# Kernel tuning notes

Hardware: AMD Instinct MI355X
Metric: run time of the kernel (lower is better)

## Reference

```python
import jax, jax.numpy as jnp
import numpy as np

# dims: batch, num queries, context len, model dim, heads, head dim,
# num_q_group, v_repeat, lora rank
B, NQ, NC, D = 4, 416, 257, 768
H, DH = 6, 128
G, R, LORA = 104, 4, 64  # NQ == R * G, all_q_mid == G * LORA
EPS = 1e-5


def ln(x, g, b):
    m = jnp.mean(x, axis=-1, keepdims=True)
    v = jnp.mean(jnp.square(x - m), axis=-1, keepdims=True)
    return (x - m) * jax.lax.rsqrt(v + EPS) * g + b


def setup_inputs() -> dict:
    key = jax.random.key(0)
    ks = jax.random.split(key, 7)
    s = 0.02
    return {
        "x": jax.random.normal(ks[0], (B, NQ, D), dtype=jnp.float32),
        "context": jax.random.normal(ks[1], (B, NC, D), dtype=jnp.float32),
        "Wq": jax.random.normal(ks[2], (D, D), dtype=jnp.float32) * s,
        "gq": jnp.ones((D,), jnp.float32), "bq": jnp.zeros((D,), jnp.float32),
        "Wk": jax.random.normal(ks[3], (D, D), dtype=jnp.float32) * s,
        "gk": jnp.ones((D,), jnp.float32), "bk": jnp.zeros((D,), jnp.float32),
        "Wv": jax.random.normal(ks[4], (D, G * LORA), dtype=jnp.float32) * s,
        "gv1": jnp.ones((G * LORA,), jnp.float32), "bv1": jnp.zeros((G * LORA,), jnp.float32),
        "Wconv": jax.random.normal(ks[5], (G, LORA, D), dtype=jnp.float32) * s,  # grouped 1x1 conv: per-group (LORA -> D)
        "gv2": jnp.ones((D,), jnp.float32), "bv2": jnp.zeros((D,), jnp.float32),
        "Wo": jax.random.normal(ks[6], (D, D), dtype=jnp.float32) * s,
        "go": jnp.ones((D,), jnp.float32), "bo": jnp.zeros((D,), jnp.float32),
    }


def reference(x, context, Wq, gq, bq, Wk, gk, bk, Wv, gv1, bv1, Wconv, gv2, bv2, Wo, go, bo):
    # to_q / to_k: Linear (no bias) + affine LayerNorm
    q = ln(x @ Wq, gq, bq)          # (B, NQ, D)
    k = ln(context @ Wk, gk, bk)    # (B, NC, D)
    # split heads -> (B*H, n, DH)
    q = q.reshape(B, NQ, H, DH).transpose(0, 2, 1, 3).reshape(B * H, NQ, DH)
    k = k.reshape(B, NC, H, DH).transpose(0, 2, 1, 3).reshape(B * H, NC, DH)

    # q-aware to_v: Linear -> LN -> grouped 1x1 Conv1d -> LN, plus skip of context
    mid = ln(context @ Wv, gv1, bv1)                 # (B, NC, G*LORA)
    mid = mid.reshape(B, NC, G, LORA)
    v = jnp.einsum('bngl,gld->bgnd', mid, Wconv)     # grouped conv, (B, G, NC, D)
    v = ln(v, gv2, bv2)
    v = v + context[:, None]                          # v_has_skip: context.unsqueeze(1)
    # heads: (B, G, NC, H, DH) -> (B*H, G, NC, DH)
    v = v.reshape(B, G, NC, H, DH).transpose(0, 3, 1, 2, 4).reshape(B * H, G, NC, DH)

    scale = DH ** (-0.25)
    sim = jnp.einsum('bid,bjd->bij', q * scale, k * scale)   # (B*H, NQ, NC)
    attn = jax.nn.softmax(sim, axis=-1)                       # dropout in eval mode: identity

    # torch repeat(1, R, 1, 1) tiles v along q-dim: query i uses group i % G.
    # reshape attn to (B*H, R, G, NC) so that i = r*G + g maps to group g.
    attn_g = attn.reshape(B * H, R, G, NC)
    out = jnp.einsum('brgj,bgjd->brgd', attn_g, v).reshape(B * H, NQ, DH)

    # merge heads -> (B, NQ, D)
    out = out.reshape(B, H, NQ, DH).transpose(0, 2, 1, 3).reshape(B, NQ, D)
    # to_out: Linear (no bias) + Dropout(eval: identity) + affine LayerNorm
    return ln(out @ Wo, go, bo)
```

## Files before the change

kernel.cpp:

```cpp
#include <hip/hip_runtime.h>


typedef unsigned short u16;
typedef unsigned int   u32;
typedef __attribute__((ext_vector_type(4))) float f32x4;
typedef __attribute__((ext_vector_type(4))) u32   u32x4;
typedef __attribute__((ext_vector_type(8))) short bf16x8;

__device__ __forceinline__ float bf2f(u16 v) { return __uint_as_float(((u32)v) << 16); }
__device__ __forceinline__ u16 f2bf(float f) {
  u32 u = __float_as_uint(f);
  u32 r = u + 0x7fffu + ((u >> 16) & 1u);
  return (u16)(r >> 16);
}
__device__ __forceinline__ float gld(const void* p, long idx, int f32) {
  return f32 ? ((const float*)p)[idx] : bf2f(((const u16*)p)[idx]);
}

typedef const __attribute__((address_space(1))) u32 gas_u32;
typedef __attribute__((address_space(3))) u32 las_u32;

__device__ __forceinline__ void stage16(const u16* g, u16* lbase, int lane) {
#if __has_builtin(__builtin_amdgcn_global_load_lds)
  (void)lane;
  __builtin_amdgcn_global_load_lds((gas_u32*)g, (las_u32*)lbase, 16, 0, 0);
#else
  *(u32x4*)(lbase + lane * 8) = *(const u32x4*)g;
#endif
}

__global__ __launch_bounds__(256) void probe_k(const u32* __restrict__ xw, int* __restrict__ flag) {
  int tid = threadIdx.x, c = 0;
  for (int i = tid; i < 4096; i += 256) {
    u16 lo = (u16)(xw[i] & 0xffffu);
    float a = fabsf(bf2f(lo));
    if (lo == 0 || (a >= 1e-3f && a <= 32.f)) ++c;
  }
#pragma unroll
  for (int o = 32; o; o >>= 1) c += __shfl_xor(c, o, 64);
  __shared__ int r[4];
  if ((tid & 63) == 0) r[tid >> 6] = c;
  __syncthreads();
  if (tid == 0) flag[0] = (r[0] + r[1] + r[2] + r[3] >= 2048) ? 0 : 1;
}

__global__ __launch_bounds__(256) void fill_k(u16* p, float v, int n) {
  int i = blockIdx.x * 256 + threadIdx.x;
  if (i < n) p[i] = f2bf(v);
}

__global__ __launch_bounds__(256) void prep_k(
    const void* __restrict__ x,   u16* __restrict__ xb,
    const void* __restrict__ ctx, u16* __restrict__ cbuf,
    const void* __restrict__ Wcv, u16* __restrict__ wcvb,
    u16* __restrict__ midi,
    const void* __restrict__ Wq, const void* __restrict__ Wk,
    const void* __restrict__ Wo, const void* __restrict__ Wv,
    u16* __restrict__ wqt, u16* __restrict__ wkt, u16* __restrict__ wot,
    u16* __restrict__ wvt, u16* __restrict__ ctxT,
    float* __restrict__ wbar, const int* __restrict__ dtf)
{
  const int f = dtf[0];
  int bid = blockIdx.x;
  __shared__ float s[32][33];
  if (bid < 3597) {
    const long n0_ = 1277952, n1_ = 789504, n2_ = 5111808, n3_ = 186368;
    long i = ((long)bid * 256 + threadIdx.x) * 8;
    const long t0 = n0_, t1 = t0 + n1_, t2 = t1 + n2_, t3 = t2 + n3_;
    if (i >= t3) return;
    if (i >= t2) {
      long e = i - t2;
      long z = e / 448, off = e - z * 448;
      u32x4 zz = {0u, 0u, 0u, 0u};
      *(u32x4*)(midi + z * 16896 + 16448 + off) = zz;
      return;
    }
    const void* in; u16* out;
    if (i < t0)      { in = x;    out = xb; }
    else if (i < t1) { in = ctx;  out = cbuf; i -= t0; }
    else             { in = Wcv;  out = wcvb; i -= t1; }
    if (f) {
      const float* ip = (const float*)in + i;
      f32x4 a = *(const f32x4*)ip, b = *(const f32x4*)(ip + 4);
      u32x4 q = { (u32)f2bf(a.x) | ((u32)f2bf(a.y) << 16),
                  (u32)f2bf(a.z) | ((u32)f2bf(a.w) << 16),
                  (u32)f2bf(b.x) | ((u32)f2bf(b.y) << 16),
                  (u32)f2bf(b.z) | ((u32)f2bf(b.w) << 16) };
      *(u32x4*)(out + i) = q;
    } else {
      *(u32x4*)(out + i) = *(const u32x4*)((const u16*)in + i);
    }
  } else if (bid < 11181) {
    int t = bid - 3597;
    const void* in; u16* out;
    int inK, inN, ldo, outK, nx;
    long inBase = 0, outBase = 0;
    if (t < 1728) {
      int w = t / 576; t -= w * 576;
      in  = w == 0 ? Wq : w == 1 ? Wk : Wo;
      out = w == 0 ? wqt : w == 1 ? wkt : wot;
      inK = 768; inN = 768; ldo = 768; outK = 768; nx = 24;
    } else if (t < 6720) {
      t -= 1728;
      in = Wv; out = wvt;
      inK = 768; inN = 6656; ldo = 768; outK = 768; nx = 208;
    } else {
      t -= 6720;
      int b = t / 216; t -= b * 216;
      in = ctx; out = ctxT;
      inK = 257; inN = 768; ldo = 264; outK = 264; nx = 24;
      inBase = (long)b * 257 * 768; outBase = (long)b * 768 * 264;
    }
    int n0 = (t % nx) * 32, k0 = (t / nx) * 32;
    int tx = threadIdx.x & 31, ty = threadIdx.x >> 5;
#pragma unroll
    for (int i = 0; i < 32; i += 8) {
      int k = k0 + ty + i, n = n0 + tx;
      float v = 0.f;
      if (k < inK && n < inN) v = gld(in, inBase + (long)k * inN + n, f);
      s[ty + i][tx] = v;
    }
    __syncthreads();
#pragma unroll
    for (int i = 0; i < 32; i += 8) {
      int n = n0 + ty + i, k = k0 + tx;
      if (n < inN && k < outK) out[outBase + (long)n * ldo + k] = f2bf(s[tx][ty + i]);
    }
  } else {
    int r = (bid - 11181) * 4 + (threadIdx.x >> 6);
    int lane = threadIdx.x & 63;
    long base = (long)r * 768;
    float sm = 0.f;
    for (int c = lane; c < 768; c += 64) sm += gld(Wcv, base + c, f);
#pragma unroll
    for (int o = 32; o; o >>= 1) sm += __shfl_xor(sm, o, 64);
    if (lane == 0) wbar[r] = sm * (1.f / 768.f);
  }
}

__device__ __forceinline__ void gemm128_body(
    const u16* __restrict__ A, const u16* __restrict__ B, u16* __restrict__ C,
    int M, int N, int K, int lda, int ldb, int ldc, int m0, int n0)
{
  __shared__ __attribute__((aligned(16))) u16 As[128 * 32];
  __shared__ __attribute__((aligned(16))) u16 Bs[128 * 32];
  const int tid = threadIdx.x, lane = tid & 63, wave = tid >> 6;
  const int wm = (wave >> 1) * 64, wn = (wave & 1) * 64;
  const int fm = lane & 15, fq = lane >> 4;

  const int srow = lane >> 2, selem = (lane & 3) * 8;
  int ra1 = m0 + wave * 16 + srow;      if (ra1 > M - 1) ra1 = M - 1;
  int ra2 = m0 + 64 + wave * 16 + srow; if (ra2 > M - 1) ra2 = M - 1;
  const int rb1 = n0 + wave * 16 + srow;
  const int rb2 = n0 + 64 + wave * 16 + srow;
  const u16* pa1 = A + (long)ra1 * lda + selem;
  const u16* pa2 = A + (long)ra2 * lda + selem;
  const u16* pb1 = B + (long)rb1 * ldb + selem;
  const u16* pb2 = B + (long)rb2 * ldb + selem;
  u16* la1 = As + wave * 512;
  u16* la2 = As + 2048 + wave * 512;
  u16* lb1 = Bs + wave * 512;
  u16* lb2 = Bs + 2048 + wave * 512;

  f32x4 acc[4][4];
  const f32x4 zero4 = {0.f, 0.f, 0.f, 0.f};
#pragma unroll
  for (int a_ = 0; a_ < 4; ++a_)
#pragma unroll
    for (int b_ = 0; b_ < 4; ++b_) acc[a_][b_] = zero4;

  for (int k0 = 0; k0 < K; k0 += 32) {
    stage16(pa1, la1, lane);
    stage16(pa2, la2, lane);
    stage16(pb1, lb1, lane);
    stage16(pb2, lb2, lane);
    pa1 += 32; pa2 += 32; pb1 += 32; pb2 += 32;
    __syncthreads();
    bf16x8 fa[4], fb[4];
#pragma unroll
    for (int mt = 0; mt < 4; ++mt)
      fa[mt] = *(const bf16x8*)&As[(wm + mt * 16 + fm) * 32 + fq * 8];
#pragma unroll
    for (int nt = 0; nt < 4; ++nt)
      fb[nt] = *(const bf16x8*)&Bs[(wn + nt * 16 + fm) * 32 + fq * 8];
#pragma unroll
    for (int mt = 0; mt < 4; ++mt)
#pragma unroll
      for (int nt = 0; nt < 4; ++nt)
        acc[mt][nt] = __builtin_amdgcn_mfma_f32_16x16x32_bf16(fa[mt], fb[nt], acc[mt][nt], 0, 0, 0);
    __syncthreads();
  }
#pragma unroll
  for (int mt = 0; mt < 4; ++mt)
#pragma unroll
    for (int nt = 0; nt < 4; ++nt)
#pragma unroll
      for (int rr = 0; rr < 4; ++rr) {
        int gm = m0 + wm + mt * 16 + fq * 4 + rr;
        int gn = n0 + wn + nt * 16 + fm;
        if (gm < M) C[(long)gm * ldc + gn] = f2bf(acc[mt][nt][rr]);
      }
}

__global__ __launch_bounds__(256) void gemm128(
    const u16* __restrict__ A, const u16* __restrict__ B, u16* __restrict__ C,
    int M, int N, int K, int lda, int ldb, int ldc)
{
  gemm128_body(A, B, C, M, N, K, lda, ldb, ldc, blockIdx.x * 128, blockIdx.y * 128);
}

#define LDS_S 40

__device__ __forceinline__ void gemm64_body(
    u16* As, u16* Bs,
    const u16* __restrict__ A16, const u16* __restrict__ B16,
    float* Cf, u16* Cb, float* Ylds,
    int M, int N, int K, int lda, int ldb, int ldc,
    int btrans, float alpha, int m0, int n0)
{
  const int tid = threadIdx.x;
  const int lane = tid & 63, wave = tid >> 6;
  const int wm = (wave >> 1) * 32, wn = (wave & 1) * 32;
  const int fm = lane & 15, fq = lane >> 4;
  const int ar = tid >> 2, ak = (tid & 3) * 8;
  const int bk = tid >> 3, bn = (tid & 7) * 8;

  f32x4 acc[2][2];
  const f32x4 zero4 = {0.f, 0.f, 0.f, 0.f};
#pragma unroll
  for (int a_ = 0; a_ < 2; ++a_)
#pragma unroll
    for (int b_ = 0; b_ < 2; ++b_) acc[a_][b_] = zero4;

  for (int k0 = 0; k0 < K; k0 += 32) {
    {
      int gm = m0 + ar, gk = k0 + ak;
      long idx = (long)gm * lda + gk;
      if (gm < M && gk + 8 <= K) {
        *(u32x4*)&As[ar * LDS_S + ak] = *(const u32x4*)(A16 + idx);
      } else {
#pragma unroll
        for (int e = 0; e < 8; ++e)
          As[ar * LDS_S + ak + e] = (gm < M && gk + e < K) ? A16[idx + e] : (u16)0;
      }
    }
    if (btrans) {
      int gn = n0 + ar, gk = k0 + ak;
      long idx = (long)gn * ldb + gk;
      if (gn < N && gk + 8 <= K) {
        *(u32x4*)&Bs[ar * LDS_S + ak] = *(const u32x4*)(B16 + idx);
      } else {
#pragma unroll
        for (int e = 0; e < 8; ++e)
          Bs[ar * LDS_S + ak + e] = (gn < N && gk + e < K) ? B16[idx + e] : (u16)0;
      }
    } else {
      int gk = k0 + bk;
      long idx = (long)gk * ldb + n0 + bn;
      u16 tmp[8];
      if (gk < K) {
        u32x4 v = *(const u32x4*)(B16 + idx);
        tmp[0] = (u16)(v.x & 0xffff); tmp[1] = (u16)(v.x >> 16);
        tmp[2] = (u16)(v.y & 0xffff); tmp[3] = (u16)(v.y >> 16);
        tmp[4] = (u16)(v.z & 0xffff); tmp[5] = (u16)(v.z >> 16);
        tmp[6] = (u16)(v.w & 0xffff); tmp[7] = (u16)(v.w >> 16);
      } else {
#pragma unroll
        for (int e = 0; e < 8; ++e) tmp[e] = 0;
      }
      int rot = tid & 7;
#pragma unroll
      for (int e = 0; e < 8; ++e) {
        int ee = (e + rot) & 7;
        Bs[(bn + ee) * LDS_S + bk] = tmp[ee];
      }
    }
    __syncthreads();
    {
      bf16x8 fa[2], fb[2];
      fa[0] = *(const bf16x8*)&As[(wm +      fm) * LDS_S + fq * 8];
      fa[1] = *(const bf16x8*)&As[(wm + 16 + fm) * LDS_S + fq * 8];
      fb[0] = *(const bf16x8*)&Bs[(wn +      fm) * LDS_S + fq * 8];
      fb[1] = *(const bf16x8*)&Bs[(wn + 16 + fm) * LDS_S + fq * 8];
#pragma unroll
      for (int mt = 0; mt < 2; ++mt)
#pragma unroll
        for (int nt = 0; nt < 2; ++nt)
          acc[mt][nt] = __builtin_amdgcn_mfma_f32_16x16x32_bf16(fa[mt], fb[nt], acc[mt][nt], 0, 0, 0);
    }
    __syncthreads();
  }
  if (Ylds) {
#pragma unroll
    for (int mt = 0; mt < 2; ++mt)
#pragma unroll
      for (int nt = 0; nt < 2; ++nt)
#pragma unroll
        for (int rr = 0; rr < 4; ++rr)
          Ylds[(wm + mt * 16 + fq * 4 + rr) * 64 + (wn + nt * 16 + fm)] = acc[mt][nt][rr];
  } else {
#pragma unroll
    for (int mt = 0; mt < 2; ++mt)
#pragma unroll
      for (int nt = 0; nt < 2; ++nt)
#pragma unroll
        for (int rr = 0; rr < 4; ++rr) {
          int gm = m0 + wm + mt * 16 + fq * 4 + rr;
          int gn = n0 + wn + nt * 16 + fm;
          if (gm < M && gn < N) {
            float v = alpha * acc[mt][nt][rr];
            if (Cb) Cb[(long)gm * ldc + gn] = f2bf(v);
            else    Cf[(long)gm * ldc + gn] = v;
          }
        }
  }
}

__global__ __launch_bounds__(256) void mg4_k(
    const u16* __restrict__ xb, const u16* __restrict__ wqt, u16* __restrict__ qbf,
    const u16* __restrict__ cbuf, const u16* __restrict__ wkt, u16* __restrict__ kbf,
    const u16* __restrict__ wvt, u16* __restrict__ midbf,
    const u16* __restrict__ wcvb, u16* __restrict__ Gb)
{
  int bid = blockIdx.x;
  if (bid < 600) {
    const u16 *A, *B; u16* C; int M, N, lid, mx;
    if (bid < 78)       { A = xb;   B = wqt; C = qbf;   M = 1664; N = 768;  lid = bid;       mx = 13; }
    else if (bid < 132) { A = cbuf; B = wkt; C = kbf;   M = 1028; N = 768;  lid = bid - 78;  mx = 9;  }
    else                { A = cbuf; B = wvt; C = midbf; M = 1028; N = 6656; lid = bid - 132; mx = 9;  }
    int m0 = (lid % mx) * 128, n0 = (lid / mx) * 128;
    gemm128_body(A, B, C, M, N, 768, 768, 768, N, m0, n0);
  } else {
    __shared__ __attribute__((aligned(16))) u16 As[64 * LDS_S];
    __shared__ __attribute__((aligned(16))) u16 Bs[64 * LDS_S];
    int z = bid - 600;
    gemm64_body(As, Bs, wcvb + (long)z * 49152, wcvb + (long)z * 49152,
                nullptr, Gb + (long)z * 4096, nullptr,
                64, 64, 768, 768, 768, 64, 1, 1.f / 768.f, 0, 0);
  }
}

__global__ __launch_bounds__(256) void ysim_k(
    const u16* __restrict__ midbf, const u16* __restrict__ Gb,
    const float* __restrict__ wbar, u16* __restrict__ midi, float* __restrict__ pim,
    const u16* __restrict__ qbf, const u16* __restrict__ kbf, float* __restrict__ simf)
{
  __shared__ __attribute__((aligned(16))) char smem[16384];
  u16* As = (u16*)smem;
  u16* Bs = (u16*)(smem + 8192);
  int bid = blockIdx.x;
  if (bid < 1768) {
    int g = bid / 17, bx = bid % 17;
    int m0 = bx * 64;
    float* Ylds = (float*)smem;
    gemm64_body(As, Bs, midbf + (long)g * 64, Gb + (long)g * 4096,
                nullptr, nullptr, Ylds,
                1028, 64, 64, 6656, 64, 64, 1, 1.f, m0, 0);
    __syncthreads();
    int tid = threadIdx.x, lane = tid & 63, wave = tid >> 6;
#pragma unroll
    for (int rr = 0; rr < 16; ++rr) {
      int r = wave * 16 + rr;
      int gr = m0 + r;
      if (gr < 1028) {
        float m  = bf2f(midbf[(long)gr * 6656 + g * 64 + lane]);
        float y  = Ylds[r * 64 + lane];
        float wb = wbar[g * 64 + lane];
        float mup = m * wb, q2p = m * y;
#pragma unroll
        for (int o = 32; o; o >>= 1) { mup += __shfl_xor(mup, o, 64); q2p += __shfl_xor(q2p, o, 64); }
        float var = q2p - mup * mup;
        float inv = rsqrtf(fmaxf(var, 0.f) + 1e-5f);
        int b = gr / 257, j = gr - b * 257;
        long zidx = (long)b * 104 + g;
        midi[(zidx * 264 + j) * 64 + lane] = f2bf(inv * m);
        if (lane == 0) pim[zidx * 257 + j] = inv * mup;
      }
    }
  } else {
    int lid = bid - 1768; int z = lid / 35, r = lid % 35, bx = r % 7, by = r / 7;
    const u16* A = qbf + (long)(z / 6) * 319488 + (long)(z % 6) * 128;
    const u16* B = kbf + (long)(z / 6) * 197376 + (long)(z % 6) * 128;
    float* Cf = simf + (long)z * 106912;
    gemm64_body(As, Bs, A, B, Cf, nullptr, nullptr,
                416, 257, 128, 768, 768, 257, 1, 0.08838834764831845f, bx * 64, by * 64);
  }
}

__global__ __launch_bounds__(256) void ct_k(
    const u16* __restrict__ Abf, const u16* __restrict__ ctxT, float* __restrict__ c_buf,
    const u16* __restrict__ A2bf, const u16* __restrict__ midi, u16* __restrict__ Tb16)
{
  __shared__ __attribute__((aligned(16))) u16 As[64 * LDS_S];
  __shared__ __attribute__((aligned(16))) u16 Bs[64 * LDS_S];
  int bid = blockIdx.x;
  if (bid < 336) {
    int z = bid / 14, r = bid % 14, bx = r % 7, by = r / 7;
    const u16* A = Abf + (long)z * 109824;
    const u16* B = ctxT + (long)(z / 6) * 202752 + (long)(z % 6) * 33792;
    float* Cf = c_buf + (long)z * 53248;
    gemm64_body(As, Bs, A, B, Cf, nullptr, nullptr,
                416, 128, 264, 264, 264, 128, 1, 1.f, bx * 64, by * 64);
  } else {
    int z = bid - 336;
    const u16* A = A2bf + (long)z * 6336;
    const u16* B = midi + (long)z * 16896;
    u16* Cb = Tb16 + (long)z * 1536;
    gemm64_body(As, Bs, A, B, nullptr, Cb, nullptr,
                24, 64, 264, 264, 64, 64, 0, 1.f, 0, 0);
  }
}

__device__ __forceinline__ void ln_row(
    const u16* __restrict__ ip, const void* __restrict__ g, const void* __restrict__ b,
    u16* __restrict__ ob, float* __restrict__ of, int N, int f)
{
  int tid = threadIdx.x, lane = tid & 63, wave = tid >> 6;
  const int nv = N >> 3;
  float s1 = 0.f, s2 = 0.f;
  for (int c8 = tid; c8 < nv; c8 += 256) {
    u32x4 v = *(const u32x4*)(ip + c8 * 8);
    float e0 = bf2f((u16)(v.x & 0xffff)), e1 = bf2f((u16)(v.x >> 16));
    float e2 = bf2f((u16)(v.y & 0xffff)), e3 = bf2f((u16)(v.y >> 16));
    float e4 = bf2f((u16)(v.z & 0xffff)), e5 = bf2f((u16)(v.z >> 16));
    float e6 = bf2f((u16)(v.w & 0xffff)), e7 = bf2f((u16)(v.w >> 16));
    s1 += ((e0 + e1) + (e2 + e3)) + ((e4 + e5) + (e6 + e7));
    s2 += ((e0*e0 + e1*e1) + (e2*e2 + e3*e3)) + ((e4*e4 + e5*e5) + (e6*e6 + e7*e7));
  }
#pragma unroll
  for (int o = 32; o; o >>= 1) { s1 += __shfl_xor(s1, o, 64); s2 += __shfl_xor(s2, o, 64); }
  __shared__ float red[8];
  if (lane == 0) { red[wave] = s1; red[4 + wave] = s2; }
  __syncthreads();
  s1 = red[0] + red[1] + red[2] + red[3];
  s2 = red[4] + red[5] + red[6] + red[7];
  float mean = s1 / N;
  float var = s2 / N - mean * mean;
  float rstd = rsqrtf(fmaxf(var, 0.f) + 1e-5f);
  for (int c8 = tid; c8 < nv; c8 += 256) {
    int c = c8 * 8;
    u32x4 v = *(const u32x4*)(ip + c);
    float e[8];
    e[0] = bf2f((u16)(v.x & 0xffff)); e[1] = bf2f((u16)(v.x >> 16));
    e[2] = bf2f((u16)(v.y & 0xffff)); e[3] = bf2f((u16)(v.y >> 16));
    e[4] = bf2f((u16)(v.z & 0xffff)); e[5] = bf2f((u16)(v.z >> 16));
    e[6] = bf2f((u16)(v.w & 0xffff)); e[7] = bf2f((u16)(v.w >> 16));
    float gg[8], bb[8];
    if (f) {
      const float* gp = (const float*)g + c; const float* bp = (const float*)b + c;
      f32x4 g0 = *(const f32x4*)gp, g1 = *(const f32x4*)(gp + 4);
      f32x4 b0 = *(const f32x4*)bp, b1 = *(const f32x4*)(bp + 4);
      gg[0]=g0.x; gg[1]=g0.y; gg[2]=g0.z; gg[3]=g0.w; gg[4]=g1.x; gg[5]=g1.y; gg[6]=g1.z; gg[7]=g1.w;
      bb[0]=b0.x; bb[1]=b0.y; bb[2]=b0.z; bb[3]=b0.w; bb[4]=b1.x; bb[5]=b1.y; bb[6]=b1.z; bb[7]=b1.w;
    } else {
      u32x4 gv = *(const u32x4*)((const u16*)g + c);
      u32x4 bv = *(const u32x4*)((const u16*)b + c);
      gg[0]=bf2f((u16)(gv.x&0xffff)); gg[1]=bf2f((u16)(gv.x>>16));
      gg[2]=bf2f((u16)(gv.y&0xffff)); gg[3]=bf2f((u16)(gv.y>>16));
      gg[4]=bf2f((u16)(gv.z&0xffff)); gg[5]=bf2f((u16)(gv.z>>16));
      gg[6]=bf2f((u16)(gv.w&0xffff)); gg[7]=bf2f((u16)(gv.w>>16));
      bb[0]=bf2f((u16)(bv.x&0xffff)); bb[1]=bf2f((u16)(bv.x>>16));
      bb[2]=bf2f((u16)(bv.y&0xffff)); bb[3]=bf2f((u16)(bv.y>>16));
      bb[4]=bf2f((u16)(bv.z&0xffff)); bb[5]=bf2f((u16)(bv.z>>16));
      bb[6]=bf2f((u16)(bv.w&0xffff)); bb[7]=bf2f((u16)(bv.w>>16));
    }
    float o_[8];
#pragma unroll
    for (int e2i = 0; e2i < 8; ++e2i) o_[e2i] = (e[e2i] - mean) * rstd * gg[e2i] + bb[e2i];
    if (of) {
      f32x4 o0 = {o_[0], o_[1], o_[2], o_[3]}, o1 = {o_[4], o_[5], o_[6], o_[7]};
      *(f32x4*)(of + c) = o0; *(f32x4*)(of + c + 4) = o1;
    } else {
      u32x4 q = { (u32)f2bf(o_[0]) | ((u32)f2bf(o_[1]) << 16),
                  (u32)f2bf(o_[2]) | ((u32)f2bf(o_[3]) << 16),
                  (u32)f2bf(o_[4]) | ((u32)f2bf(o_[5]) << 16),
                  (u32)f2bf(o_[6]) | ((u32)f2bf(o_[7]) << 16) };
      *(u32x4*)(ob + c) = q;
    }
  }
}

__global__ __launch_bounds__(256) void ln_rows(
    const u16* __restrict__ in, const void* __restrict__ g, const void* __restrict__ b,
    void* __restrict__ out, int N, const int* __restrict__ dtf, int isfinal)
{
  const int f = dtf[0];
  long row = blockIdx.x;
  const u16* ip = in + row * N;
  float* of = (isfinal && f) ? (float*)out + row * N : nullptr;
  u16*   ob = of ? nullptr : (u16*)out + row * N;
  ln_row(ip, g, b, ob, of, N, f);
}

__global__ __launch_bounds__(256) void mln3_k(
    u16* __restrict__ qb, const void* __restrict__ gq, const void* __restrict__ bq,
    u16* __restrict__ kb, const void* __restrict__ gk, const void* __restrict__ bk,
    u16* __restrict__ mb, const void* __restrict__ gv, const void* __restrict__ bv,
    const int* __restrict__ dtf)
{
  const int f = dtf[0];
  int row = blockIdx.x;
  u16* ip; const void *g, *b; int N;
  if (row < 1664)      { ip = qb + (long)row * 768; g = gq; b = bq; N = 768; }
  else if (row < 2692) { ip = kb + (long)(row - 1664) * 768; g = gk; b = bk; N = 768; }
  else                 { ip = mb + (long)(row - 2692) * 6656; g = gv; b = bv; N = 6656; }
  ln_row(ip, g, b, ip, nullptr, N, f);
}

__global__ __launch_bounds__(256) void softmax_k(
    const float* __restrict__ simf, const float* __restrict__ pim,
    u16* __restrict__ Abf, u16* __restrict__ A2bf, float* __restrict__ s_sh)
{
  int bh = blockIdx.x;
  int b = bh / 6, h = bh - b * 6;
  int tid = threadIdx.x, lane = tid & 63, wave = tid >> 6;
  int i = blockIdx.y * 4 + wave;
  int g = i % 104, rq = i / 104;
  const float* sp_ = simf + ((long)bh * 416 + i) * 257;
  float s[5];
#pragma unroll
  for (int jc = 0; jc < 5; ++jc) {
    int j = jc * 64 + lane;
    s[jc] = (j < 257) ? sp_[j] : -1e30f;
  }
  float mx = -1e30f;
#pragma unroll
  for (int jc = 0; jc < 5; ++jc) mx = fmaxf(mx, s[jc]);
#pragma unroll
  for (int o = 32; o; o >>= 1) mx = fmaxf(mx, __shfl_xor(mx, o, 64));
  float p[5], sum = 0.f, sp = 0.f;
  long pimb = ((long)b * 104 + g) * 257;
#pragma unroll
  for (int jc = 0; jc < 5; ++jc) {
    int j = jc * 64 + lane;
    float pv = 0.f;
    if (j < 257) { pv = __expf(s[jc] - mx); sp = fmaf(pv, pim[pimb + j], sp); }
    p[jc] = pv; sum += pv;
  }
#pragma unroll
  for (int o = 32; o; o >>= 1) { sum += __shfl_xor(sum, o, 64); sp += __shfl_xor(sp, o, 64); }
  float rs = 1.f / sum;
  long arow  = ((long)bh * 416 + i) * 264;
  long a2row = (((long)b * 104 + g) * 24 + h * 4 + rq) * 264;
#pragma unroll
  for (int jc = 0; jc < 5; ++jc) {
    int j = jc * 64 + lane;
    if (j < 257) { u16 pb = f2bf(p[jc] * rs); Abf[arow + j] = pb; A2bf[a2row + j] = pb; }
    else if (j < 264) { Abf[arow + j] = 0; A2bf[a2row + j] = 0; }
  }
  if (lane == 0) s_sh[(long)bh * 416 + i] = sp * rs;
}

__global__ __launch_bounds__(256) void oc_k(
    const u16* __restrict__ T, const u16* __restrict__ Wb,
    const float* __restrict__ s_sh, const float* __restrict__ c_buf,
    const void* __restrict__ gv2, const void* __restrict__ bv2,
    u16* __restrict__ opbf, const int* __restrict__ dtf)
{
  const int f = dtf[0];
  int z = blockIdx.x;
  int b = z / 104, g = z - b * 104;
  int tid = threadIdx.x;
  __shared__ float Ts[24][64];
  const u16* tp = T + (long)z * 1536;
  for (int idx = tid; idx < 1536; idx += 256) Ts[idx >> 6][idx & 63] = bf2f(tp[idx]);
  __syncthreads();
  const int dh = tid & 127;
  const int hbase = (tid >> 7) * 3;
  const u16* wg = Wb + (long)g * 49152;
#pragma unroll
  for (int hh = 0; hh < 3; ++hh) {
    int h = hbase + hh;
    int d = h * 128 + dh;
    const u16* wp = wg + d;
    float a0 = 0.f, a1 = 0.f, a2 = 0.f, a3 = 0.f;
#pragma unroll 16
    for (int k = 0; k < 64; ++k) {
      float w = bf2f(wp[(long)k * 768]);
      a0 = fmaf(Ts[h * 4 + 0][k], w, a0);
      a1 = fmaf(Ts[h * 4 + 1][k], w, a1);
      a2 = fmaf(Ts[h * 4 + 2][k], w, a2);
      a3 = fmaf(Ts[h * 4 + 3][k], w, a3);
    }
    float acc[4] = {a0, a1, a2, a3};
    float gvd = gld(gv2, d, f), bvd = gld(bv2, d, f);
#pragma unroll
    for (int rq = 0; rq < 4; ++rq) {
      int i = rq * 104 + g;
      float ssh = s_sh[((long)b * 6 + h) * 416 + i];
      float val = gvd * (acc[rq] - ssh) + bvd
                + c_buf[(((long)b * 6 + h) * 416 + i) * 128 + dh];
      opbf[((long)b * 416 + i) * 768 + d] = f2bf(val);
    }
  }
}

extern "C" void kernel_launch(void* const* d_in, const int* in_sizes, int n_in,
                              void* d_out, int out_size, void* d_ws, size_t ws_size,
                              hipStream_t stream)
{
  (void)in_sizes; (void)n_in;
  const void* x   = d_in[0];
  const void* ctx = d_in[1];
  const void* Wq  = d_in[2];
  const void* gq  = d_in[3];
  const void* bq  = d_in[4];
  const void* Wk  = d_in[5];
  const void* gk  = d_in[6];
  const void* bk  = d_in[7];
  const void* Wv  = d_in[8];
  const void* gv1 = d_in[9];
  const void* bv1 = d_in[10];
  const void* Wcv = d_in[11];
  const void* gv2 = d_in[12];
  const void* bv2 = d_in[13];
  const void* Wo  = d_in[14];
  const void* go  = d_in[15];
  const void* bo  = d_in[16];

  const size_t SZ_FLAG = 256;
  const size_t SZ_QBF  = 2555904;
  const size_t SZ_KBF  = 1579008;
  const size_t SZ_MID  = 13684736;
  const size_t SZ_MM   = 1703936;
  const size_t SZ_WB   = 26624;
  const size_t SZ_MIDI = 14057472;
  const size_t SZ_PIM  = 427648;
  const size_t SZ_ABF  = 5271552;
  const size_t SZ_A2   = 5271552;
  const size_t SZ_SSH  = 39936;
  const size_t SZ_CB   = 1579008;
  const size_t SZ_WCVB = 10223616;
  const size_t SZ_WT   = 1179648;
  const size_t SZ_WVT  = 10223616;
  const size_t SZ_CTXT = 1622016;
  const size_t SZ_SIMF = 10263552;
  const size_t REQUIRED = SZ_FLAG + SZ_QBF + SZ_KBF + SZ_MID + SZ_MM + SZ_WB +
                          SZ_MIDI + SZ_PIM + SZ_ABF + SZ_A2 + SZ_SSH + SZ_CB +
                          SZ_WCVB + 3 * SZ_WT + SZ_WVT + SZ_CTXT + SZ_SIMF;

  if (ws_size < REQUIRED) {
    fill_k<<<(out_size + 255) / 256, 256, 0, stream>>>((u16*)d_out, (float)(ws_size >> 20), out_size);
    return;
  }

  char* p = (char*)d_ws;
  int*   dtf   = (int*)  p;                 p += SZ_FLAG;
  u16*   qbf   = (u16*)  p;                 p += SZ_QBF;
  u16*   kbf   = (u16*)  p;                 p += SZ_KBF;
  char*  midrg = p;                         p += SZ_MID;
  char*  mmrg  = p;                         p += SZ_MM;
  float* wbar  = (float*)p;                 p += SZ_WB;
  u16*   midi  = (u16*)  p;                 p += SZ_MIDI;
  float* pim   = (float*)p;                 p += SZ_PIM;
  char*  abfrg = p;                         p += SZ_ABF;
  u16*   A2bf  = (u16*)  p;                 p += SZ_A2;
  float* s_sh  = (float*)p;                 p += SZ_SSH;
  u16*   cb    = (u16*)  p;                 p += SZ_CB;
  u16*   wcvb  = (u16*)  p;                 p += SZ_WCVB;
  u16*   wqt2  = (u16*)  p;                 p += SZ_WT;
  u16*   wkt2  = (u16*)  p;                 p += SZ_WT;
  u16*   wot2  = (u16*)  p;                 p += SZ_WT;
  u16*   wvt   = (u16*)  p;                 p += SZ_WVT;
  u16*   ctxT  = (u16*)  p;                 p += SZ_CTXT;
  float* simf  = (float*)p;                 p += SZ_SIMF;

  u16*   midbf = (u16*)midrg;
  float* c_buf = (float*)midrg;
  u16*   Tb16  = (u16*)(midrg + 5111808);
  u16*   Gb    = (u16*)mmrg;
  u16*   xb    = (u16*)abfrg;
  u16*   Abf   = (u16*)abfrg;
  u16*   opbf  = (u16*)abfrg;

  probe_k<<<1, 256, 0, stream>>>((const u32*)x, dtf);

  prep_k<<<12845, 256, 0, stream>>>(x, xb, ctx, cb, Wcv, wcvb, midi,
                                    Wq, Wk, Wo, Wv, wqt2, wkt2, wot2, wvt, ctxT,
                                    wbar, dtf);

  mg4_k<<<704, 256, 0, stream>>>(xb, wqt2, qbf, cb, wkt2, kbf, wvt, midbf, wcvb, Gb);

  mln3_k<<<3720, 256, 0, stream>>>(qbf, gq, bq, kbf, gk, bk, midbf, gv1, bv1, dtf);

  ysim_k<<<2608, 256, 0, stream>>>(midbf, Gb, wbar, midi, pim, qbf, kbf, simf);

  softmax_k<<<dim3(24, 104), 256, 0, stream>>>(simf, pim, Abf, A2bf, s_sh);

  ct_k<<<752, 256, 0, stream>>>(Abf, ctxT, c_buf, A2bf, midi, Tb16);

  oc_k<<<416, 256, 0, stream>>>(Tb16, wcvb, s_sh, c_buf, gv2, bv2, opbf, dtf);

  {
    dim3 grid(13, 6, 1);
    gemm128<<<grid, dim3(256), 0, stream>>>(opbf, wot2, qbf, 1664, 768, 768, 768, 768, 768);
  }
  ln_rows<<<1664, 256, 0, stream>>>(qbf, go, bo, d_out, 768, dtf, 1);
}
```

Baseline: 262.9 us.

## Fuse QK^T sim GEMM with softmax and move wbar/pim-dot into other kernels

Replaces the separate sim GEMM (fp32 sim buffer written to global) and softmax kernel with one simsm_k kernel. It computes a 32-row tile of QK^T into LDS and applies softmax in place, writing bf16 probabilities directly. The wbar row-mean moves from prep_k into mg4_k and reads the already-converted bf16 Wconv. The pim-weighted sum moves to extra blocks in ct_k. This removes the ~10MB fp32 sim round trip and one launch, but simsm_k has only 312 blocks with large LDS (about 60KB), which may leave the GPU underfilled.

```diff
diff --git a/kernel.cpp b/kernel.cpp
--- a/kernel.cpp
+++ b/kernel.cpp
@@ -58,7 +58,7 @@
     const void* __restrict__ Wo, const void* __restrict__ Wv,
     u16* __restrict__ wqt, u16* __restrict__ wkt, u16* __restrict__ wot,
     u16* __restrict__ wvt, u16* __restrict__ ctxT,
-    float* __restrict__ wbar, const int* __restrict__ dtf)
+    const int* __restrict__ dtf)
 {
   const int f = dtf[0];
   int bid = blockIdx.x;
@@ -90,7 +90,7 @@
     } else {
       *(u32x4*)(out + i) = *(const u32x4*)((const u16*)in + i);
     }
-  } else if (bid < 11181) {
+  } else {
     int t = bid - 3597;
     const void* in; u16* out;
     int inK, inN, ldo, outK, nx;
@@ -126,15 +126,6 @@
       int n = n0 + ty + i, k = k0 + tx;
       if (n < inN && k < outK) out[outBase + (long)n * ldo + k] = f2bf(s[tx][ty + i]);
     }
-  } else {
-    int r = (bid - 11181) * 4 + (threadIdx.x >> 6);
-    int lane = threadIdx.x & 63;
-    long base = (long)r * 768;
-    float sm = 0.f;
-    for (int c = lane; c < 768; c += 64) sm += gld(Wcv, base + c, f);
-#pragma unroll
-    for (int o = 32; o; o >>= 1) sm += __shfl_xor(sm, o, 64);
-    if (lane == 0) wbar[r] = sm * (1.f / 768.f);
   }
 }
 
@@ -320,7 +311,7 @@
     const u16* __restrict__ xb, const u16* __restrict__ wqt, u16* __restrict__ qbf,
     const u16* __restrict__ cbuf, const u16* __restrict__ wkt, u16* __restrict__ kbf,
     const u16* __restrict__ wvt, u16* __restrict__ midbf,
-    const u16* __restrict__ wcvb, u16* __restrict__ Gb)
+    const u16* __restrict__ wcvb, u16* __restrict__ Gb, float* __restrict__ wbar)
 {
   int bid = blockIdx.x;
   if (bid < 600) {
@@ -330,84 +321,197 @@
     else                { A = cbuf; B = wvt; C = midbf; M = 1028; N = 6656; lid = bid - 132; mx = 9;  }
     int m0 = (lid % mx) * 128, n0 = (lid / mx) * 128;
     gemm128_body(A, B, C, M, N, 768, 768, 768, N, m0, n0);
-  } else {
+  } else if (bid < 704) {
     __shared__ __attribute__((aligned(16))) u16 As[64 * LDS_S];
     __shared__ __attribute__((aligned(16))) u16 Bs[64 * LDS_S];
     int z = bid - 600;
     gemm64_body(As, Bs, wcvb + (long)z * 49152, wcvb + (long)z * 49152,
                 nullptr, Gb + (long)z * 4096, nullptr,
                 64, 64, 768, 768, 768, 64, 1, 1.f / 768.f, 0, 0);
+  } else {
+    int r = (bid - 704) * 4 + (threadIdx.x >> 6);
+    int lane = threadIdx.x & 63;
+    const u16* prow = wcvb + (long)r * 768;
+    float sm = 0.f;
+    for (int c = lane; c < 768; c += 64) sm += bf2f(prow[c]);
+#pragma unroll
+    for (int o = 32; o; o >>= 1) sm += __shfl_xor(sm, o, 64);
+    if (lane == 0) wbar[r] = sm * (1.f / 768.f);
   }
 }
 
 __global__ __launch_bounds__(256) void ysim_k(
     const u16* __restrict__ midbf, const u16* __restrict__ Gb,
-    const float* __restrict__ wbar, u16* __restrict__ midi, float* __restrict__ pim,
-    const u16* __restrict__ qbf, const u16* __restrict__ kbf, float* __restrict__ simf)
+    const float* __restrict__ wbar, u16* __restrict__ midi, float* __restrict__ pim)
 {
   __shared__ __attribute__((aligned(16))) char smem[16384];
   u16* As = (u16*)smem;
   u16* Bs = (u16*)(smem + 8192);
   int bid = blockIdx.x;
-  if (bid < 1768) {
-    int g = bid / 17, bx = bid % 17;
-    int m0 = bx * 64;
-    float* Ylds = (float*)smem;
-    gemm64_body(As, Bs, midbf + (long)g * 64, Gb + (long)g * 4096,
-                nullptr, nullptr, Ylds,
-                1028, 64, 64, 6656, 64, 64, 1, 1.f, m0, 0);
+  int g = bid / 17, bx = bid % 17;
+  int m0 = bx * 64;
+  float* Ylds = (float*)smem;
+  gemm64_body(As, Bs, midbf + (long)g * 64, Gb + (long)g * 4096,
+              nullptr, nullptr, Ylds,
+              1028, 64, 64, 6656, 64, 64, 1, 1.f, m0, 0);
+  __syncthreads();
+  int tid = threadIdx.x, lane = tid & 63, wave = tid >> 6;
+#pragma unroll
+  for (int rr = 0; rr < 16; ++rr) {
+    int r = wave * 16 + rr;
+    int gr = m0 + r;
+    if (gr < 1028) {
+      float m  = bf2f(midbf[(long)gr * 6656 + g * 64 + lane]);
+      float y  = Ylds[r * 64 + lane];
+      float wb = wbar[g * 64 + lane];
+      float mup = m * wb, q2p = m * y;
+#pragma unroll
+      for (int o = 32; o; o >>= 1) { mup += __shfl_xor(mup, o, 64); q2p += __shfl_xor(q2p, o, 64); }
+      float var = q2p - mup * mup;
+      float inv = rsqrtf(fmaxf(var, 0.f) + 1e-5f);
+      int b = gr / 257, j = gr - b * 257;
+      long zidx = (long)b * 104 + g;
+      midi[(zidx * 264 + j) * 64 + lane] = f2bf(inv * m);
+      if (lane == 0) pim[zidx * 257 + j] = inv * mup;
+    }
+  }
+}
+
+#define SS 136
+
+__global__ __launch_bounds__(256) void simsm_k(
+    const u16* __restrict__ qbf, const u16* __restrict__ kbf,
+    u16* __restrict__ Abf, u16* __restrict__ A2bf)
+{
+  __shared__ __attribute__((aligned(16))) u16 Aq[32 * SS];
+  __shared__ __attribute__((aligned(16))) u16 Bk[64 * SS];
+  __shared__ float S[32 * 264];
+  int bid = blockIdx.x;
+  int z = bid / 13, mt = bid - z * 13;
+  int b = z / 6, h = z - b * 6;
+  int m0 = mt * 32;
+  int tid = threadIdx.x, lane = tid & 63, wave = tid >> 6;
+  const int fm = lane & 15, fq = lane >> 4;
+  const int wm = (wave >> 1) * 16, wn = (wave & 1) * 32;
+  const float alpha = 0.08838834764831845f;
+
+  const u16* qb = qbf + (long)b * 319488 + h * 128;
+  for (int ch = tid; ch < 512; ch += 256) {
+    int row = ch >> 4, c8 = (ch & 15) * 8;
+    *(u32x4*)&Aq[row * SS + c8] = *(const u32x4*)(qb + (long)(m0 + row) * 768 + c8);
+  }
+  const u16* kb = kbf + (long)b * 197376 + h * 128;
+
+  for (int jt = 0; jt < 5; ++jt) {
+    int j0 = jt * 64;
     __syncthreads();
-    int tid = threadIdx.x, lane = tid & 63, wave = tid >> 6;
-#pragma unroll
-    for (int rr = 0; rr < 16; ++rr) {
-      int r = wave * 16 + rr;
-      int gr = m0 + r;
-      if (gr < 1028) {
-        float m  = bf2f(midbf[(long)gr * 6656 + g * 64 + lane]);
-        float y  = Ylds[r * 64 + lane];
-        float wb = wbar[g * 64 + lane];
-        float mup = m * wb, q2p = m * y;
-#pragma unroll
-        for (int o = 32; o; o >>= 1) { mup += __shfl_xor(mup, o, 64); q2p += __shfl_xor(q2p, o, 64); }
-        float var = q2p - mup * mup;
-        float inv = rsqrtf(fmaxf(var, 0.f) + 1e-5f);
-        int b = gr / 257, j = gr - b * 257;
-        long zidx = (long)b * 104 + g;
-        midi[(zidx * 264 + j) * 64 + lane] = f2bf(inv * m);
-        if (lane == 0) pim[zidx * 257 + j] = inv * mup;
-      }
-    }
-  } else {
-    int lid = bid - 1768; int z = lid / 35, r = lid % 35, bx = r % 7, by = r / 7;
-    const u16* A = qbf + (long)(z / 6) * 319488 + (long)(z % 6) * 128;
-    const u16* B = kbf + (long)(z / 6) * 197376 + (long)(z % 6) * 128;
-    float* Cf = simf + (long)z * 106912;
-    gemm64_body(As, Bs, A, B, Cf, nullptr, nullptr,
-                416, 257, 128, 768, 768, 257, 1, 0.08838834764831845f, bx * 64, by * 64);
+    for (int ch = tid; ch < 1024; ch += 256) {
+      int row = ch >> 4, c8 = (ch & 15) * 8;
+      int j = j0 + row; if (j > 256) j = 256;
+      *(u32x4*)&Bk[row * SS + c8] = *(const u32x4*)(kb + (long)j * 768 + c8);
+    }
+    __syncthreads();
+    f32x4 acc[2];
+    acc[0] = (f32x4){0.f, 0.f, 0.f, 0.f};
+    acc[1] = (f32x4){0.f, 0.f, 0.f, 0.f};
+#pragma unroll
+    for (int ks = 0; ks < 4; ++ks) {
+      bf16x8 fa = *(const bf16x8*)&Aq[(wm + fm) * SS + ks * 32 + fq * 8];
+#pragma unroll
+      for (int nt = 0; nt < 2; ++nt) {
+        bf16x8 fb = *(const bf16x8*)&Bk[(wn + nt * 16 + fm) * SS + ks * 32 + fq * 8];
+        acc[nt] = __builtin_amdgcn_mfma_f32_16x16x32_bf16(fa, fb, acc[nt], 0, 0, 0);
+      }
+    }
+#pragma unroll
+    for (int nt = 0; nt < 2; ++nt)
+#pragma unroll
+      for (int rr = 0; rr < 4; ++rr) {
+        int col = j0 + wn + nt * 16 + fm;
+        if (col < 264) S[(wm + fq * 4 + rr) * 264 + col] = acc[nt][rr];
+      }
+  }
+  __syncthreads();
+  for (int rr = 0; rr < 8; ++rr) {
+    int il = wave * 8 + rr;
+    int i = m0 + il;
+    int g = i % 104, rq = i / 104;
+    float s[5];
+#pragma unroll
+    for (int c = 0; c < 5; ++c) {
+      int j = c * 64 + lane;
+      s[c] = (j < 257) ? S[il * 264 + j] * alpha : -1e30f;
+    }
+    float mx = -1e30f;
+#pragma unroll
+    for (int c = 0; c < 5; ++c) mx = fmaxf(mx, s[c]);
+#pragma unroll
+    for (int o = 32; o; o >>= 1) mx = fmaxf(mx, __shfl_xor(mx, o, 64));
+    float p[5], sum = 0.f;
+#pragma unroll
+    for (int c = 0; c < 5; ++c) {
+      int j = c * 64 + lane;
+      p[c] = (j < 257) ? __expf(s[c] - mx) : 0.f;
+      sum += p[c];
+    }
+#pragma unroll
+    for (int o = 32; o; o >>= 1) sum += __shfl_xor(sum, o, 64);
+    float rs = 1.f / sum;
+    long arow  = ((long)z * 416 + i) * 264;
+    long a2row = (((long)b * 104 + g) * 24 + h * 4 + rq) * 264;
+#pragma unroll
+    for (int c = 0; c < 5; ++c) {
+      int j = c * 64 + lane;
+      if (j < 257) { u16 pb = f2bf(p[c] * rs); Abf[arow + j] = pb; A2bf[a2row + j] = pb; }
+      else if (j < 264) { Abf[arow + j] = 0; A2bf[a2row + j] = 0; }
+    }
   }
 }
 
 __global__ __launch_bounds__(256) void ct_k(
     const u16* __restrict__ Abf, const u16* __restrict__ ctxT, float* __restrict__ c_buf,
-    const u16* __restrict__ A2bf, const u16* __restrict__ midi, u16* __restrict__ Tb16)
-{
-  __shared__ __attribute__((aligned(16))) u16 As[64 * LDS_S];
-  __shared__ __attribute__((aligned(16))) u16 Bs[64 * LDS_S];
+    const u16* __restrict__ A2bf, const u16* __restrict__ midi, u16* __restrict__ Tb16,
+    const float* __restrict__ pim, float* __restrict__ s_sh)
+{
   int bid = blockIdx.x;
   if (bid < 336) {
+    __shared__ __attribute__((aligned(16))) u16 As[64 * LDS_S];
+    __shared__ __attribute__((aligned(16))) u16 Bs[64 * LDS_S];
     int z = bid / 14, r = bid % 14, bx = r % 7, by = r / 7;
     const u16* A = Abf + (long)z * 109824;
     const u16* B = ctxT + (long)(z / 6) * 202752 + (long)(z % 6) * 33792;
     float* Cf = c_buf + (long)z * 53248;
     gemm64_body(As, Bs, A, B, Cf, nullptr, nullptr,
                 416, 128, 264, 264, 264, 128, 1, 1.f, bx * 64, by * 64);
-  } else {
+  } else if (bid < 752) {
+    __shared__ __attribute__((aligned(16))) u16 As[64 * LDS_S];
+    __shared__ __attribute__((aligned(16))) u16 Bs[64 * LDS_S];
     int z = bid - 336;
     const u16* A = A2bf + (long)z * 6336;
     const u16* B = midi + (long)z * 16896;
     u16* Cb = Tb16 + (long)z * 1536;
     gemm64_body(As, Bs, A, B, nullptr, Cb, nullptr,
                 24, 64, 264, 264, 64, 64, 0, 1.f, 0, 0);
+  } else {
+    int z = bid - 752;
+    int b = z / 104, g = z - b * 104;
+    int lane = threadIdx.x & 63, wave = threadIdx.x >> 6;
+    const u16* a2 = A2bf + (long)z * 6336;
+    const float* pz = pim + (long)z * 257;
+    for (int r = wave; r < 24; r += 4) {
+      float sp = 0.f;
+#pragma unroll
+      for (int c = 0; c < 5; ++c) {
+        int j = c * 64 + lane;
+        if (j < 257) sp = fmaf(bf2f(a2[r * 264 + j]), pz[j], sp);
+      }
+#pragma unroll
+      for (int o = 32; o; o >>= 1) sp += __shfl_xor(sp, o, 64);
+      if (lane == 0) {
+        int h = r >> 2, rq = r & 3;
+        s_sh[((long)b * 6 + h) * 416 + rq * 104 + g] = sp;
+      }
+    }
   }
 }
 
@@ -507,50 +611,6 @@
   ln_row(ip, g, b, ip, nullptr, N, f);
 }
 
-__global__ __launch_bounds__(256) void softmax_k(
-    const float* __restrict__ simf, const float* __restrict__ pim,
-    u16* __restrict__ Abf, u16* __restrict__ A2bf, float* __restrict__ s_sh)
-{
-  int bh = blockIdx.x;
-  int b = bh / 6, h = bh - b * 6;
-  int tid = threadIdx.x, lane = tid & 63, wave = tid >> 6;
-  int i = blockIdx.y * 4 + wave;
-  int g = i % 104, rq = i / 104;
-  const float* sp_ = simf + ((long)bh * 416 + i) * 257;
-  float s[5];
-#pragma unroll
-  for (int jc = 0; jc < 5; ++jc) {
-    int j = jc * 64 + lane;
-    s[jc] = (j < 257) ? sp_[j] : -1e30f;
-  }
-  float mx = -1e30f;
-#pragma unroll
-  for (int jc = 0; jc < 5; ++jc) mx = fmaxf(mx, s[jc]);
-#pragma unroll
-  for (int o = 32; o; o >>= 1) mx = fmaxf(mx, __shfl_xor(mx, o, 64));
-  float p[5], sum = 0.f, sp = 0.f;
-  long pimb = ((long)b * 104 + g) * 257;
-#pragma unroll
-  for (int jc = 0; jc < 5; ++jc) {
-    int j = jc * 64 + lane;
-    float pv = 0.f;
-    if (j < 257) { pv = __expf(s[jc] - mx); sp = fmaf(pv, pim[pimb + j], sp); }
-    p[jc] = pv; sum += pv;
-  }
-#pragma unroll
-  for (int o = 32; o; o >>= 1) { sum += __shfl_xor(sum, o, 64); sp += __shfl_xor(sp, o, 64); }
-  float rs = 1.f / sum;
-  long arow  = ((long)bh * 416 + i) * 264;
-  long a2row = (((long)b * 104 + g) * 24 + h * 4 + rq) * 264;
-#pragma unroll
-  for (int jc = 0; jc < 5; ++jc) {
-    int j = jc * 64 + lane;
-    if (j < 257) { u16 pb = f2bf(p[jc] * rs); Abf[arow + j] = pb; A2bf[a2row + j] = pb; }
-    else if (j < 264) { Abf[arow + j] = 0; A2bf[a2row + j] = 0; }
-  }
-  if (lane == 0) s_sh[(long)bh * 416 + i] = sp * rs;
-}
-
 __global__ __launch_bounds__(256) void oc_k(
     const u16* __restrict__ T, const u16* __restrict__ Wb,
     const float* __restrict__ s_sh, const float* __restrict__ c_buf,
@@ -634,10 +694,9 @@
   const size_t SZ_WT   = 1179648;
   const size_t SZ_WVT  = 10223616;
   const size_t SZ_CTXT = 1622016;
-  const size_t SZ_SIMF = 10263552;
   const size_t REQUIRED = SZ_FLAG + SZ_QBF + SZ_KBF + SZ_MID + SZ_MM + SZ_WB +
                           SZ_MIDI + SZ_PIM + SZ_ABF + SZ_A2 + SZ_SSH + SZ_CB +
-                          SZ_WCVB + 3 * SZ_WT + SZ_WVT + SZ_CTXT + SZ_SIMF;
+                          SZ_WCVB + 3 * SZ_WT + SZ_WVT + SZ_CTXT;
 
   if (ws_size < REQUIRED) {
     fill_k<<<(out_size + 255) / 256, 256, 0, stream>>>((u16*)d_out, (float)(ws_size >> 20), out_size);
@@ -663,7 +722,6 @@
   u16*   wot2  = (u16*)  p;                 p += SZ_WT;
   u16*   wvt   = (u16*)  p;                 p += SZ_WVT;
   u16*   ctxT  = (u16*)  p;                 p += SZ_CTXT;
-  float* simf  = (float*)p;                 p += SZ_SIMF;
 
   u16*   midbf = (u16*)midrg;
   float* c_buf = (float*)midrg;
@@ -675,19 +733,20 @@
 
   probe_k<<<1, 256, 0, stream>>>((const u32*)x, dtf);
 
-  prep_k<<<12845, 256, 0, stream>>>(x, xb, ctx, cb, Wcv, wcvb, midi,
+  prep_k<<<11181, 256, 0, stream>>>(x, xb, ctx, cb, Wcv, wcvb, midi,
                                     Wq, Wk, Wo, Wv, wqt2, wkt2, wot2, wvt, ctxT,
-                                    wbar, dtf);
-
-  mg4_k<<<704, 256, 0, stream>>>(xb, wqt2, qbf, cb, wkt2, kbf, wvt, midbf, wcvb, Gb);
+                                    dtf);
+
+  mg4_k<<<2368, 256, 0, stream>>>(xb, wqt2, qbf, cb, wkt2, kbf, wvt, midbf,
+                                  wcvb, Gb, wbar);
 
   mln3_k<<<3720, 256, 0, stream>>>(qbf, gq, bq, kbf, gk, bk, midbf, gv1, bv1, dtf);
 
-  ysim_k<<<2608, 256, 0, stream>>>(midbf, Gb, wbar, midi, pim, qbf, kbf, simf);
-
-  softmax_k<<<dim3(24, 104), 256, 0, stream>>>(simf, pim, Abf, A2bf, s_sh);
-
-  ct_k<<<752, 256, 0, stream>>>(Abf, ctxT, c_buf, A2bf, midi, Tb16);
+  ysim_k<<<1768, 256, 0, stream>>>(midbf, Gb, wbar, midi, pim);
+
+  simsm_k<<<312, 256, 0, stream>>>(qbf, kbf, Abf, A2bf);
+
+  ct_k<<<1168, 256, 0, stream>>>(Abf, ctxT, c_buf, A2bf, midi, Tb16, pim, s_sh);
 
   oc_k<<<416, 256, 0, stream>>>(Tb16, wcvb, s_sh, c_buf, gv2, bv2, opbf, dtf);
 
```

Result: slower. 276.3 us (+5.1%).
